# Performance work log

Hardware: AMD Instinct MI355X
Metric: run time of the kernel (lower is better)

The kernel has to match this reference:

```python
import jax, jax.numpy as jnp
import numpy as np
import math

HIDDEN = 1024
HEADS = 16
HEAD_DIM = HIDDEN // HEADS
B, S = 4, 2048


def setup_inputs() -> dict:
    key = jax.random.key(0)
    ks = jax.random.split(key, 9)
    std = 1.0 / math.sqrt(HIDDEN)
    return {
        "query": jax.random.normal(ks[0], (B, S, HIDDEN), jnp.float32),
        "key": jax.random.normal(ks[1], (B, S, HIDDEN), jnp.float32),
        "value": jax.random.normal(ks[2], (B, S, HIDDEN), jnp.float32),
        "q_w": jax.random.normal(ks[3], (HIDDEN, HIDDEN), jnp.float32) * std,
        "q_b": jax.random.normal(ks[4], (HIDDEN,), jnp.float32) * 0.02,
        "k_w": jax.random.normal(ks[5], (HIDDEN, HIDDEN), jnp.float32) * std,
        "k_b": jax.random.normal(ks[6], (HIDDEN,), jnp.float32) * 0.02,
        "v_w": jax.random.normal(ks[7], (HIDDEN, HIDDEN), jnp.float32) * std,
        "v_b": jax.random.normal(ks[8], (HIDDEN,), jnp.float32) * 0.02,
    }


def _split_heads(x):
    # [B, S, H] -> [B, heads, S, head_dim]
    b, s, _ = x.shape
    return x.reshape(b, s, HEADS, HEAD_DIM).transpose(0, 2, 1, 3)


def reference(query, key, value, q_w, q_b, k_w, k_b, v_w, v_b):
    # Linear projections (torch Linear: x @ W^T + b; here weights stored as [in, out])
    q = _split_heads(query @ q_w + q_b)   # [B, h, S, d]
    k = _split_heads(key @ k_w + k_b)
    v = _split_heads(value @ v_w + v_b)
    scale = 1.0 / math.sqrt(HEAD_DIM)
    scores = jnp.einsum("bhqd,bhkd->bhqk", q, k) * scale  # [B, h, S, S]
    # NOTE: faithful to source bug — context uses raw scaled scores, NOT softmax probs.
    # (softmax is computed in the original but its result is unused for the output.)
    ctx = jnp.einsum("bhqk,bhkd->bhqd", scores, v)
    ctx = ctx.transpose(0, 2, 1, 3).reshape(query.shape[0], query.shape[1], HIDDEN)
    return ctx
```

## Files before the change

### kernel.cpp

```cpp
#include <hip/hip_runtime.h>
#include <stdint.h>

#define HIDDEN 1024
#define HEADS 16
#define HEAD_DIM 64
#define BATCH 4
#define SEQ 2048
#define ROWS (BATCH * SEQ)

typedef float f32x4 __attribute__((ext_vector_type(4)));
typedef short bf16x8 __attribute__((ext_vector_type(8)));

__device__ __forceinline__ uint16_t f32_to_bf16_rne(float f) {
    uint32_t u = __float_as_uint(f);
    uint32_t r = u + 0x7FFFu + ((u >> 16) & 1u);
    return (uint16_t)(r >> 16);
}
__device__ __forceinline__ float bf16_to_f32(uint16_t u) {
    return __uint_as_float(((uint32_t)u) << 16);
}

__global__ __launch_bounds__(256) void cvt_kernel(const float* __restrict__ Xq,
                                                  const float* __restrict__ Xk,
                                                  const float* __restrict__ Xv,
                                                  uint16_t* __restrict__ Xb) {
    int z = blockIdx.x >> 12;
    const float* X = z == 0 ? Xq : (z == 1 ? Xk : Xv);
    uint16_t* out = Xb + (size_t)z * ROWS * HIDDEN;
    size_t e = ((size_t)(blockIdx.x & 4095) * 256 + threadIdx.x) * 8;
    float4 f0 = *(const float4*)(X + e);
    float4 f1 = *(const float4*)(X + e + 4);
    uint4 pk;
    pk.x = (uint32_t)f32_to_bf16_rne(f0.x) | ((uint32_t)f32_to_bf16_rne(f0.y) << 16);
    pk.y = (uint32_t)f32_to_bf16_rne(f0.z) | ((uint32_t)f32_to_bf16_rne(f0.w) << 16);
    pk.z = (uint32_t)f32_to_bf16_rne(f1.x) | ((uint32_t)f32_to_bf16_rne(f1.y) << 16);
    pk.w = (uint32_t)f32_to_bf16_rne(f1.z) | ((uint32_t)f32_to_bf16_rne(f1.w) << 16);
    *(uint4*)(out + e) = pk;
}

__global__ __launch_bounds__(256) void wt_kernel(const float* __restrict__ Wk,
                                                 const float* __restrict__ Wv,
                                                 uint16_t* __restrict__ Wt) {
    const float* W = blockIdx.z == 0 ? Wk : Wv;
    uint16_t* out = Wt + (size_t)blockIdx.z * HIDDEN * HIDDEN;
    __shared__ float tile[64][65];
    int k0 = blockIdx.x * 64, n0 = blockIdx.y * 64;
    int r = threadIdx.x >> 6, c = threadIdx.x & 63;
    for (int it = 0; it < 16; ++it) {
        int rr = r + 4 * it;
        tile[rr][c] = W[(size_t)(k0 + rr) * HIDDEN + n0 + c];
    }
    __syncthreads();
    for (int it = 0; it < 16; ++it) {
        int rr = r + 4 * it;
        out[(size_t)(n0 + rr) * HIDDEN + k0 + c] = f32_to_bf16_rne(tile[c][rr]);
    }
}

__global__ __launch_bounds__(256) void proj_gemm(const uint16_t* __restrict__ Xkv,
                                                 const uint16_t* __restrict__ Wt,
                                                 const float* __restrict__ Bk,
                                                 const float* __restrict__ Bv,
                                                 uint16_t* __restrict__ KV) {
    const int z = blockIdx.z;
    const uint16_t* X = Xkv + (size_t)z * ROWS * HIDDEN;
    const uint16_t* W = Wt + (size_t)z * HIDDEN * HIDDEN;
    const float* bias = z == 0 ? Bk : Bv;
    uint16_t* out = KV + (size_t)z * ROWS * HIDDEN;

    __shared__ uint16_t lds[16384];

    const int tid = threadIdx.x;
    const int lane = tid & 63;
    const int w = tid >> 6;
    const int wm = (w >> 1) * 64;
    const int wn = (w & 1) * 64;
    const int m_lane = lane & 15;
    const int kq = lane >> 4;
    const int m0 = blockIdx.x * 128;
    const int n0 = blockIdx.y * 128;

    f32x4 acc[4][4] = {};

    for (int kb = 0; kb < HIDDEN; kb += 64) {
        for (int t = 0; t < 4; ++t) {
            int gbase = (w * 4 + t) * 64;
            int g = gbase + lane;
            int r = g >> 3;
            int c = (g & 7) ^ (r & 7);
            const uint16_t* srcA = X + (size_t)(m0 + r) * HIDDEN + kb + c * 8;
            __builtin_amdgcn_global_load_lds(
                (const __attribute__((address_space(1))) uint32_t*)srcA,
                (__attribute__((address_space(3))) uint32_t*)(&lds[gbase * 8]),
                16, 0, 0);
            const uint16_t* srcB = W + (size_t)(n0 + r) * HIDDEN + kb + c * 8;
            __builtin_amdgcn_global_load_lds(
                (const __attribute__((address_space(1))) uint32_t*)srcB,
                (__attribute__((address_space(3))) uint32_t*)(&lds[8192 + gbase * 8]),
                16, 0, 0);
        }
        __syncthreads();
        for (int ks = 0; ks < 2; ++ks) {
            int cbase = ks * 4 + kq;
            bf16x8 af[4], bfr[4];
            for (int i = 0; i < 4; ++i) {
                int r = wm + i * 16 + m_lane;
                int p = cbase ^ (r & 7);
                af[i] = *(const bf16x8*)(&lds[r * 64 + p * 8]);
            }
            for (int j = 0; j < 4; ++j) {
                int nr = wn + j * 16 + m_lane;
                int p = cbase ^ (nr & 7);
                bfr[j] = *(const bf16x8*)(&lds[8192 + nr * 64 + p * 8]);
            }
            for (int i = 0; i < 4; ++i)
                for (int j = 0; j < 4; ++j)
                    acc[i][j] = __builtin_amdgcn_mfma_f32_16x16x32_bf16(
                        af[i], bfr[j], acc[i][j], 0, 0, 0);
        }
        __syncthreads();
    }

    for (int j = 0; j < 4; ++j) {
        int col = n0 + wn + j * 16 + m_lane;
        float bj = bias[col];
        for (int i = 0; i < 4; ++i) {
            int rbase = m0 + wm + i * 16 + kq * 4;
            for (int rg = 0; rg < 4; ++rg) {
                float v = acc[i][j][rg] + bj;
                out[(size_t)(rbase + rg) * HIDDEN + col] = f32_to_bf16_rne(v);
            }
        }
    }
}

__global__ __launch_bounds__(256) void kv_kernel(const uint16_t* __restrict__ KV,
                                                 float* __restrict__ P) {
    const uint16_t* K = KV;
    const uint16_t* V = KV + (size_t)ROWS * HIDDEN;
    const int bh = blockIdx.x;
    const int sc = blockIdx.y;
    const int b = bh >> 4, h = bh & 15;
    const int tid = threadIdx.x;
    const size_t base = ((size_t)b * SEQ + sc * 256) * HIDDEN + h * 64;

    __shared__ float kk[16][64];
    __shared__ float vv[16][64];
    float acc[4][4] = {};
    const int i0 = (tid >> 4) * 4, j0 = (tid & 15) * 4;

    for (int batch = 0; batch < 16; ++batch) {
        __syncthreads();
        {
            int t = tid & 127;
            int row = t >> 3, c = t & 7;
            const uint16_t* src =
                (tid < 128 ? K : V) + base + (size_t)(batch * 16 + row) * HIDDEN + c * 8;
            float* dst = (tid < 128 ? &kk[row][c * 8] : &vv[row][c * 8]);
            bf16x8 d = *(const bf16x8*)src;
            for (int e = 0; e < 8; ++e) dst[e] = bf16_to_f32((uint16_t)d[e]);
        }
        __syncthreads();
        for (int r = 0; r < 16; ++r) {
            f32x4 ka = *(const f32x4*)(&kk[r][i0]);
            f32x4 va = *(const f32x4*)(&vv[r][j0]);
            for (int a = 0; a < 4; ++a)
                for (int bb = 0; bb < 4; ++bb)
                    acc[a][bb] += ka[a] * va[bb];
        }
    }
    float* Pp = P + ((size_t)bh * 8 + sc) * 4096;
    for (int a = 0; a < 4; ++a) {
        f32x4 row;
        for (int bb = 0; bb < 4; ++bb) row[bb] = acc[a][bb] * 0.125f;
        *(f32x4*)(&Pp[(i0 + a) * 64 + j0]) = row;
    }
}

__global__ __launch_bounds__(256) void wprime_kernel(const float* __restrict__ Wq,
                                                     const float* __restrict__ bq,
                                                     const float* __restrict__ P,
                                                     uint16_t* __restrict__ Wpt,
                                                     float* __restrict__ bp) {
    const int h = blockIdx.x;
    const int r0 = blockIdx.y * 64;
    const int b = blockIdx.z;
    const int tid = threadIdx.x;

    __shared__ float Mh[64][65];
    __shared__ float Wl[64][65];
    const float* Pp = P + ((size_t)(b * 16 + h)) * 8 * 4096;
    for (int it = 0; it < 16; ++it) {
        int e = it * 256 + tid;
        int a = e >> 6, c = e & 63;
        float s = 0.f;
        for (int sc = 0; sc < 8; ++sc) s += Pp[sc * 4096 + e];
        Mh[a][c] = s;
        Wl[a][c] = Wq[(size_t)(r0 + a) * HIDDEN + h * 64 + c];
    }
    __syncthreads();

    const int r = tid & 63;
    const int jbase = tid >> 6;
    float acc[16] = {};
    for (int i = 0; i < 64; ++i) {
        float wv = Wl[r][i];
        for (int jj = 0; jj < 16; ++jj)
            acc[jj] += wv * Mh[i][jbase + 4 * jj];
    }
    uint16_t* Wb = Wpt + (size_t)b * HIDDEN * HIDDEN;
    for (int jj = 0; jj < 16; ++jj) {
        int n = h * 64 + jbase + 4 * jj;
        Wb[(size_t)n * HIDDEN + r0 + r] = f32_to_bf16_rne(acc[jj]);
    }

    if (blockIdx.y == 0 && tid < 64) {
        int j = tid;
        float s = 0.f;
        for (int i = 0; i < 64; ++i) s += bq[h * 64 + i] * Mh[i][j];
        bp[b * HIDDEN + h * 64 + j] = s;
    }
}

__global__ __launch_bounds__(256) void final_gemm(const uint16_t* __restrict__ Xq,
                                                  const uint16_t* __restrict__ Wpt,
                                                  const float* __restrict__ bp,
                                                  float* __restrict__ out) {
    __shared__ uint16_t lds[16384];

    const int tid = threadIdx.x;
    const int lane = tid & 63;
    const int w = tid >> 6;
    const int wm = (w >> 1) * 64;
    const int wn = (w & 1) * 64;
    const int m_lane = lane & 15;
    const int kq = lane >> 4;
    const int m0 = blockIdx.x * 128;
    const int n0 = blockIdx.y * 128;
    const int batch = m0 >> 11;
    const uint16_t* W = Wpt + (size_t)batch * HIDDEN * HIDDEN;
    const float* bias = bp + batch * HIDDEN;

    f32x4 acc[4][4] = {};

    for (int kb = 0; kb < HIDDEN; kb += 64) {
        for (int t = 0; t < 4; ++t) {
            int gbase = (w * 4 + t) * 64;
            int g = gbase + lane;
            int r = g >> 3;
            int c = (g & 7) ^ (r & 7);
            const uint16_t* srcA = Xq + (size_t)(m0 + r) * HIDDEN + kb + c * 8;
            __builtin_amdgcn_global_load_lds(
                (const __attribute__((address_space(1))) uint32_t*)srcA,
                (__attribute__((address_space(3))) uint32_t*)(&lds[gbase * 8]),
                16, 0, 0);
            const uint16_t* srcB = W + (size_t)(n0 + r) * HIDDEN + kb + c * 8;
            __builtin_amdgcn_global_load_lds(
                (const __attribute__((address_space(1))) uint32_t*)srcB,
                (__attribute__((address_space(3))) uint32_t*)(&lds[8192 + gbase * 8]),
                16, 0, 0);
        }
        __syncthreads();
        for (int ks = 0; ks < 2; ++ks) {
            int cbase = ks * 4 + kq;
            bf16x8 af[4], bfr[4];
            for (int i = 0; i < 4; ++i) {
                int r = wm + i * 16 + m_lane;
                int p = cbase ^ (r & 7);
                af[i] = *(const bf16x8*)(&lds[r * 64 + p * 8]);
            }
            for (int j = 0; j < 4; ++j) {
                int nr = wn + j * 16 + m_lane;
                int p = cbase ^ (nr & 7);
                bfr[j] = *(const bf16x8*)(&lds[8192 + nr * 64 + p * 8]);
            }
            for (int i = 0; i < 4; ++i)
                for (int j = 0; j < 4; ++j)
                    acc[i][j] = __builtin_amdgcn_mfma_f32_16x16x32_bf16(
                        af[i], bfr[j], acc[i][j], 0, 0, 0);
        }
        __syncthreads();
    }

    for (int j = 0; j < 4; ++j) {
        int col = n0 + wn + j * 16 + m_lane;
        float bj = bias[col];
        for (int i = 0; i < 4; ++i) {
            int rbase = m0 + wm + i * 16 + kq * 4;
            for (int rg = 0; rg < 4; ++rg)
                out[(size_t)(rbase + rg) * HIDDEN + col] = acc[i][j][rg] + bj;
        }
    }
}

extern "C" void kernel_launch(void* const* d_in, const int* in_sizes, int n_in,
                              void* d_out, int out_size, void* d_ws, size_t ws_size,
                              hipStream_t stream) {
    const float* Xq = (const float*)d_in[0];
    const float* Xk = (const float*)d_in[1];
    const float* Xv = (const float*)d_in[2];
    const float* Wq = (const float*)d_in[3];
    const float* Bq = (const float*)d_in[4];
    const float* Wk = (const float*)d_in[5];
    const float* Bk = (const float*)d_in[6];
    const float* Wv = (const float*)d_in[7];
    const float* Bv = (const float*)d_in[8];
    float* out = (float*)d_out;

    char* ws = (char*)d_ws;
    uint16_t* Xb = (uint16_t*)ws;
    uint16_t* KV = (uint16_t*)(ws + 50331648);
    uint16_t* Wt = (uint16_t*)(ws + 83886080);
    float* P = (float*)(ws + 88080384);
    uint16_t* Wpt = (uint16_t*)(ws + 96468992);
    float* bp = (float*)(ws + 104857600);

    cvt_kernel<<<dim3(3 * 4096), 256, 0, stream>>>(Xq, Xk, Xv, Xb);
    wt_kernel<<<dim3(16, 16, 2), 256, 0, stream>>>(Wk, Wv, Wt);

    const uint16_t* Xkv = Xb + (size_t)ROWS * HIDDEN;
    proj_gemm<<<dim3(64, 8, 2), 256, 0, stream>>>(Xkv, Wt, Bk, Bv, KV);
    kv_kernel<<<dim3(64, 8), 256, 0, stream>>>(KV, P);
    wprime_kernel<<<dim3(16, 16, 4), 256, 0, stream>>>(Wq, Bq, P, Wpt, bp);
    final_gemm<<<dim3(64, 8), 256, 0, stream>>>(Xb, Wpt, bp, out);
}
```

Before: 273.7 us.

## Rewrite K/V projection GEMM as 256x256-tile, 8-wave, double-buffered pipelined kernel

Replaces the 128x128, 4-wave projection GEMM with a 256x256 tile kernel using 512 threads and 128KB of dynamic LDS. Global-to-LDS loads for the next K-chunk are interleaved with MFMA quadrants, using explicit vmcnt waits, barriers and s_setprio. The aim is to hide load latency and raise data reuse per tile. The grid shrinks to 256 blocks, which may underfill the CUs, and the large LDS allocation limits occupancy.

```diff
diff --git a/kernel.cpp b/kernel.cpp
--- a/kernel.cpp
+++ b/kernel.cpp
@@ -57,77 +57,169 @@
     }
 }
 
-__global__ __launch_bounds__(256) void proj_gemm(const uint16_t* __restrict__ Xkv,
-                                                 const uint16_t* __restrict__ Wt,
-                                                 const float* __restrict__ Bk,
-                                                 const float* __restrict__ Bv,
-                                                 uint16_t* __restrict__ KV) {
+
+#define STAGE(GSRC, CHUNKBASE)                                                   \
+    {                                                                            \
+        _Pragma("unroll") for (int l = 0; l < 2; ++l) {                          \
+            int gb = l * 512 + w * 64;              \
+            int g = gb + lane;                                                   \
+            int r = g >> 3;                                                      \
+            int c = (g & 7) ^ (r & 7);                                           \
+            __builtin_amdgcn_global_load_lds(                                    \
+                (const __attribute__((address_space(1))) uint32_t*)((GSRC) +     \
+                    (size_t)r * HIDDEN + c * 8),                                 \
+                (__attribute__((address_space(3))) uint32_t*)(&lds[((CHUNKBASE) + gb) * 8]), \
+                16, 0, 0);                                                       \
+        }                                                                        \
+    }
+
+#define LDA(BUFU16, MH, AQ)                                                      \
+    {                                                                            \
+        _Pragma("unroll") for (int i = 0; i < 4; ++i) {                          \
+            int ar = wm + (MH) * 64 + i * 16 + m_lane;                           \
+            _Pragma("unroll") for (int ks = 0; ks < 2; ++ks) {                   \
+                int p = (ks * 4 + kq) ^ (ar & 7);                                \
+                AQ[i][ks] = *(const bf16x8*)(&lds[(BUFU16) + ar * 64 + p * 8]);  \
+            }                                                                    \
+        }                                                                        \
+    }
+
+#define LDB(BUFU16, NH, BQ)                                                      \
+    {                                                                            \
+        _Pragma("unroll") for (int j = 0; j < 2; ++j) {                          \
+            int br = wn + (NH) * 32 + j * 16 + m_lane;                           \
+            _Pragma("unroll") for (int ks = 0; ks < 2; ++ks) {                   \
+                int p = (ks * 4 + kq) ^ (br & 7);                                \
+                BQ[j][ks] = *(const bf16x8*)(&lds[(BUFU16) + 16384 + br * 64 + p * 8]); \
+            }                                                                    \
+        }                                                                        \
+    }
+
+#define MFMA_QUAD(AQ, BQ, MH, NH)                                                \
+    {                                                                            \
+        _Pragma("unroll") for (int ks = 0; ks < 2; ++ks)                         \
+        _Pragma("unroll") for (int i = 0; i < 4; ++i)                            \
+        _Pragma("unroll") for (int j = 0; j < 2; ++j)                            \
+            acc[(MH) * 4 + i][(NH) * 2 + j] =                                    \
+                __builtin_amdgcn_mfma_f32_16x16x32_bf16(                         \
+                    AQ[i][ks], BQ[j][ks], acc[(MH) * 4 + i][(NH) * 2 + j], 0, 0, 0); \
+    }
+
+#define PHASE_MID()                                                              \
+    __builtin_amdgcn_s_barrier();                                                \
+    asm volatile("s_waitcnt lgkmcnt(0)" ::: "memory");                           \
+    __builtin_amdgcn_s_setprio(1);
+
+#define PHASE_END()                                                              \
+    __builtin_amdgcn_s_setprio(0);                                               \
+    __builtin_amdgcn_s_barrier();
+
+__global__ __launch_bounds__(512, 2) void proj_gemm8(const uint16_t* __restrict__ Xkv,
+                                                     const uint16_t* __restrict__ Wt,
+                                                     const float* __restrict__ Bk,
+                                                     const float* __restrict__ Bv,
+                                                     uint16_t* __restrict__ KV) {
+    extern __shared__ uint16_t lds[];
+
     const int z = blockIdx.z;
     const uint16_t* X = Xkv + (size_t)z * ROWS * HIDDEN;
     const uint16_t* W = Wt + (size_t)z * HIDDEN * HIDDEN;
     const float* bias = z == 0 ? Bk : Bv;
     uint16_t* out = KV + (size_t)z * ROWS * HIDDEN;
 
-    __shared__ uint16_t lds[16384];
-
     const int tid = threadIdx.x;
     const int lane = tid & 63;
     const int w = tid >> 6;
-    const int wm = (w >> 1) * 64;
-    const int wn = (w & 1) * 64;
+    const int wm = (w >> 2) * 128;
+    const int wn = (w & 3) * 64;
     const int m_lane = lane & 15;
     const int kq = lane >> 4;
-    const int m0 = blockIdx.x * 128;
-    const int n0 = blockIdx.y * 128;
-
-    f32x4 acc[4][4] = {};
-
-    for (int kb = 0; kb < HIDDEN; kb += 64) {
-        for (int t = 0; t < 4; ++t) {
-            int gbase = (w * 4 + t) * 64;
-            int g = gbase + lane;
-            int r = g >> 3;
-            int c = (g & 7) ^ (r & 7);
-            const uint16_t* srcA = X + (size_t)(m0 + r) * HIDDEN + kb + c * 8;
-            __builtin_amdgcn_global_load_lds(
-                (const __attribute__((address_space(1))) uint32_t*)srcA,
-                (__attribute__((address_space(3))) uint32_t*)(&lds[gbase * 8]),
-                16, 0, 0);
-            const uint16_t* srcB = W + (size_t)(n0 + r) * HIDDEN + kb + c * 8;
-            __builtin_amdgcn_global_load_lds(
-                (const __attribute__((address_space(1))) uint32_t*)srcB,
-                (__attribute__((address_space(3))) uint32_t*)(&lds[8192 + gbase * 8]),
-                16, 0, 0);
-        }
-        __syncthreads();
-        for (int ks = 0; ks < 2; ++ks) {
-            int cbase = ks * 4 + kq;
-            bf16x8 af[4], bfr[4];
-            for (int i = 0; i < 4; ++i) {
-                int r = wm + i * 16 + m_lane;
-                int p = cbase ^ (r & 7);
-                af[i] = *(const bf16x8*)(&lds[r * 64 + p * 8]);
-            }
-            for (int j = 0; j < 4; ++j) {
-                int nr = wn + j * 16 + m_lane;
-                int p = cbase ^ (nr & 7);
-                bfr[j] = *(const bf16x8*)(&lds[8192 + nr * 64 + p * 8]);
-            }
-            for (int i = 0; i < 4; ++i)
-                for (int j = 0; j < 4; ++j)
-                    acc[i][j] = __builtin_amdgcn_mfma_f32_16x16x32_bf16(
-                        af[i], bfr[j], acc[i][j], 0, 0, 0);
-        }
-        __syncthreads();
-    }
-
-    for (int j = 0; j < 4; ++j) {
-        int col = n0 + wn + j * 16 + m_lane;
+    const int m0 = blockIdx.x * 256;
+    const int n0 = blockIdx.y * 256;
+
+    const uint16_t* Xb = X + (size_t)m0 * HIDDEN;
+    const uint16_t* Wb = W + (size_t)n0 * HIDDEN;
+
+    f32x4 acc[8][4] = {};
+    bf16x8 aq[4][2], b0q[2][2], b1q[2][2];
+
+    STAGE(Xb, 0);
+    STAGE(Xb + 128 * HIDDEN, 1024);
+    STAGE(Wb, 2048);
+    STAGE(Wb + 128 * HIDDEN, 3072);
+    STAGE(Wb + 64, 4096 + 2048);
+    STAGE(Wb + 128 * HIDDEN + 64, 4096 + 3072);
+    asm volatile("s_waitcnt vmcnt(4)" ::: "memory");
+    __builtin_amdgcn_s_barrier();
+
+#pragma unroll 1
+    for (int i = 0; i < 7; ++i) {
+        const int kb = i * 128;
+        LDA(0, 0, aq); LDB(0, 0, b0q);
+        STAGE(Xb + kb + 64, 4096 + 0);
+        PHASE_MID(); MFMA_QUAD(aq, b0q, 0, 0); PHASE_END();
+        LDB(0, 1, b1q);
+        STAGE(Xb + 128 * HIDDEN + kb + 64, 4096 + 1024);
+        PHASE_MID(); MFMA_QUAD(aq, b1q, 0, 1); PHASE_END();
+        LDA(0, 1, aq);
+        STAGE(Wb + kb + 128, 2048);
+        PHASE_MID(); MFMA_QUAD(aq, b1q, 1, 1); PHASE_END();
+        STAGE(Wb + 128 * HIDDEN + kb + 128, 3072);
+        asm volatile("s_waitcnt vmcnt(4)" ::: "memory");
+        __builtin_amdgcn_s_barrier();
+        __builtin_amdgcn_s_setprio(1);
+        MFMA_QUAD(aq, b0q, 1, 0);
+        PHASE_END();
+        LDA(32768, 0, aq); LDB(32768, 0, b0q);
+        STAGE(Xb + kb + 128, 0);
+        PHASE_MID(); MFMA_QUAD(aq, b0q, 0, 0); PHASE_END();
+        LDB(32768, 1, b1q);
+        STAGE(Xb + 128 * HIDDEN + kb + 128, 1024);
+        PHASE_MID(); MFMA_QUAD(aq, b1q, 0, 1); PHASE_END();
+        LDA(32768, 1, aq);
+        STAGE(Wb + kb + 192, 4096 + 2048);
+        PHASE_MID(); MFMA_QUAD(aq, b1q, 1, 1); PHASE_END();
+        STAGE(Wb + 128 * HIDDEN + kb + 192, 4096 + 3072);
+        asm volatile("s_waitcnt vmcnt(4)" ::: "memory");
+        __builtin_amdgcn_s_barrier();
+        __builtin_amdgcn_s_setprio(1);
+        MFMA_QUAD(aq, b0q, 1, 0);
+        PHASE_END();
+    }
+
+    {
+        const int kb = 896;
+        LDA(0, 0, aq); LDB(0, 0, b0q);
+        STAGE(Xb + kb + 64, 4096 + 0);
+        PHASE_MID(); MFMA_QUAD(aq, b0q, 0, 0); PHASE_END();
+        LDB(0, 1, b1q);
+        STAGE(Xb + 128 * HIDDEN + kb + 64, 4096 + 1024);
+        PHASE_MID(); MFMA_QUAD(aq, b1q, 0, 1); PHASE_END();
+        LDA(0, 1, aq);
+        PHASE_MID(); MFMA_QUAD(aq, b1q, 1, 1); PHASE_END();
+        asm volatile("s_waitcnt vmcnt(0)" ::: "memory");
+        __builtin_amdgcn_s_barrier();
+        __builtin_amdgcn_s_setprio(1);
+        MFMA_QUAD(aq, b0q, 1, 0);
+        PHASE_END();
+        LDA(32768, 0, aq); LDB(32768, 0, b0q);
+        PHASE_MID(); MFMA_QUAD(aq, b0q, 0, 0); PHASE_END();
+        LDB(32768, 1, b1q);
+        PHASE_MID(); MFMA_QUAD(aq, b1q, 0, 1); PHASE_END();
+        LDA(32768, 1, aq);
+        PHASE_MID(); MFMA_QUAD(aq, b1q, 1, 1); PHASE_END();
+        __builtin_amdgcn_s_setprio(1);
+        MFMA_QUAD(aq, b0q, 1, 0);
+        __builtin_amdgcn_s_setprio(0);
+    }
+
+    for (int nj = 0; nj < 4; ++nj) {
+        int col = n0 + wn + nj * 16 + m_lane;
         float bj = bias[col];
-        for (int i = 0; i < 4; ++i) {
-            int rbase = m0 + wm + i * 16 + kq * 4;
+        for (int mi = 0; mi < 8; ++mi) {
+            int rbase = m0 + wm + mi * 16 + kq * 4;
             for (int rg = 0; rg < 4; ++rg) {
-                float v = acc[i][j][rg] + bj;
+                float v = acc[mi][nj][rg] + bj;
                 out[(size_t)(rbase + rg) * HIDDEN + col] = f32_to_bf16_rne(v);
             }
         }
@@ -226,7 +318,7 @@
                                                   const uint16_t* __restrict__ Wpt,
                                                   const float* __restrict__ bp,
                                                   float* __restrict__ out) {
-    __shared__ uint16_t lds[16384];
+    __shared__ uint16_t slds[16384];
 
     const int tid = threadIdx.x;
     const int lane = tid & 63;
@@ -252,12 +344,12 @@
             const uint16_t* srcA = Xq + (size_t)(m0 + r) * HIDDEN + kb + c * 8;
             __builtin_amdgcn_global_load_lds(
                 (const __attribute__((address_space(1))) uint32_t*)srcA,
-                (__attribute__((address_space(3))) uint32_t*)(&lds[gbase * 8]),
+                (__attribute__((address_space(3))) uint32_t*)(&slds[gbase * 8]),
                 16, 0, 0);
             const uint16_t* srcB = W + (size_t)(n0 + r) * HIDDEN + kb + c * 8;
             __builtin_amdgcn_global_load_lds(
                 (const __attribute__((address_space(1))) uint32_t*)srcB,
-                (__attribute__((address_space(3))) uint32_t*)(&lds[8192 + gbase * 8]),
+                (__attribute__((address_space(3))) uint32_t*)(&slds[8192 + gbase * 8]),
                 16, 0, 0);
         }
         __syncthreads();
@@ -267,12 +359,12 @@
             for (int i = 0; i < 4; ++i) {
                 int r = wm + i * 16 + m_lane;
                 int p = cbase ^ (r & 7);
-                af[i] = *(const bf16x8*)(&lds[r * 64 + p * 8]);
+                af[i] = *(const bf16x8*)(&slds[r * 64 + p * 8]);
             }
             for (int j = 0; j < 4; ++j) {
                 int nr = wn + j * 16 + m_lane;
                 int p = cbase ^ (nr & 7);
-                bfr[j] = *(const bf16x8*)(&lds[8192 + nr * 64 + p * 8]);
+                bfr[j] = *(const bf16x8*)(&slds[8192 + nr * 64 + p * 8]);
             }
             for (int i = 0; i < 4; ++i)
                 for (int j = 0; j < 4; ++j)
@@ -315,11 +407,18 @@
     uint16_t* Wpt = (uint16_t*)(ws + 96468992);
     float* bp = (float*)(ws + 104857600);
 
+    static bool attr_done = false;
+    if (!attr_done) {
+        (void)hipFuncSetAttribute((const void*)proj_gemm8,
+                                  hipFuncAttributeMaxDynamicSharedMemorySize, 131072);
+        attr_done = true;
+    }
+
     cvt_kernel<<<dim3(3 * 4096), 256, 0, stream>>>(Xq, Xk, Xv, Xb);
     wt_kernel<<<dim3(16, 16, 2), 256, 0, stream>>>(Wk, Wv, Wt);
 
     const uint16_t* Xkv = Xb + (size_t)ROWS * HIDDEN;
-    proj_gemm<<<dim3(64, 8, 2), 256, 0, stream>>>(Xkv, Wt, Bk, Bv, KV);
+    proj_gemm8<<<dim3(32, 4, 2), 512, 131072, stream>>>(Xkv, Wt, Bk, Bv, KV);
     kv_kernel<<<dim3(64, 8), 256, 0, stream>>>(KV, P);
     wprime_kernel<<<dim3(16, 16, 4), 256, 0, stream>>>(Wq, Bq, P, Wpt, bp);
     final_gemm<<<dim3(64, 8), 256, 0, stream>>>(Xb, Wpt, bp, out);
```

Result: no change. 279.1 us (+2.0%).
